# Performance work log

Measured on AMD Instinct MI355X. Metric: run time of the kernel, lower is better.

Reference implementation:

```python
import jax, jax.numpy as jnp
import numpy as np

T, KBLK, EMB, B = 2048, 64, 512, 4


def _make_coords(t, k):
    # head1: for each j, cols = block_start(j) + arange(j % k + 1)  (block-causal local)
    j = np.arange(t)
    cnt1 = (j % k) + 1
    rows1 = np.repeat(j, cnt1)
    off1 = np.arange(cnt1.sum()) - np.repeat(np.cumsum(cnt1) - cnt1, cnt1)
    cols1 = (rows1 // k) * k + off1
    # head2: for each block start c, rows = arange(c, t), col = c  (strided block-start)
    starts = np.arange(t // k) * k
    cnt2 = t - starts
    base = np.repeat(starts, cnt2)
    off2 = np.arange(cnt2.sum()) - np.repeat(np.cumsum(cnt2) - cnt2, cnt2)
    rows2, cols2 = base + off2, base
    c1 = np.stack([rows1, cols1], 1).astype(np.int32)
    c2 = np.stack([rows2, cols2], 1).astype(np.int32)
    return c1, c2


def setup_inputs() -> dict:
    key = jax.random.key(0)
    ks = jax.random.split(key, 6)
    s = 1.0 / float(np.sqrt(EMB))
    c1, c2 = _make_coords(T, KBLK)
    return {
        "x": jax.random.normal(ks[0], (B, T, EMB), jnp.float32),
        "Wk": jax.random.normal(ks[1], (EMB, EMB), jnp.float32) * s,
        "bk": jnp.zeros((EMB,), jnp.float32),
        "Wq": jax.random.normal(ks[2], (EMB, EMB), jnp.float32) * s,
        "bq": jnp.zeros((EMB,), jnp.float32),
        "Wv": jax.random.normal(ks[3], (EMB, EMB), jnp.float32) * s,
        "bv": jnp.zeros((EMB,), jnp.float32),
        "Wu": jax.random.normal(ks[4], (EMB, 2 * EMB), jnp.float32) * s,
        "bu": jnp.zeros((EMB,), jnp.float32),
        "coords1": jnp.asarray(c1),
        "coords2": jnp.asarray(c2),
    }


def _sparse_head(Kt, Qt, Vt, coords):
    rows, cols = coords[:, 0], coords[:, 1]
    # dot[b,p] = (K @ Q^T)[b, rows[p], cols[p]] = K[b,rows[p],:] . Q[b,cols[p],:]
    dot = jnp.einsum('bpe,bpe->bp', Kt[:, rows], Qt[:, cols])
    # sparse.batchmm: out[b,r] = sum_{p: rows[p]=r} dot[b,p] * V[b, cols[p]]
    out = jnp.zeros_like(Vt).at[:, rows].add(dot[..., None] * Vt[:, cols])
    return out


def reference(x, Wk, bk, Wq, bq, Wv, bv, Wu, bu, coords1, coords2):
    Kt = x @ Wk.T + bk
    Qt = x @ Wq.T + bq
    Vt = x @ Wv.T + bv
    h1 = _sparse_head(Kt, Qt, Vt, coords1)
    h2 = _sparse_head(Kt, Qt, Vt, coords2)
    comb = jnp.concatenate([h1, h2], axis=-1)  # [B, T, 2*EMB]
    return comb @ Wu.T + bu
```

## Files before the change

kernel.cpp:

```cpp
#include <hip/hip_runtime.h>


typedef unsigned short u16;
typedef __attribute__((ext_vector_type(8))) short short8;
typedef __attribute__((ext_vector_type(4))) float f32x4;

constexpr int TDIM  = 2048;
constexpr int EMB_D = 512;
constexpr int BB    = 4;
constexpr int NBLK  = 32;
constexpr int LDK   = 2048;

__device__ __forceinline__ u16 f2b(float f) {
    unsigned u = __float_as_uint(f);
    unsigned r = (u + 0x7FFFu + ((u >> 16) & 1u)) >> 16;
    return (u16)r;
}

__global__ __launch_bounds__(256) void prep_k(
    const float* __restrict__ x, const float* __restrict__ Wk, const float* __restrict__ Wq,
    const float* __restrict__ Wv, const float* __restrict__ Wu,
    const float* __restrict__ bk, const float* __restrict__ bq, const float* __restrict__ bv,
    u16* __restrict__ xb, u16* __restrict__ wcat, float* __restrict__ biascat)
{
    const int bid = blockIdx.x, tid = threadIdx.x;
    if (bid < 32) {
        const int bm = (bid >> 2) * 128;
        const int bn = (bid & 3) * 128;
        const int wid  = tid >> 6;
        const int lane = tid & 63;
        const int l15  = lane & 15;
        const int quad = lane >> 4;
        const int wm = (wid & 1) * 64;
        const int wn = (wid >> 1) * 64;

        f32x4 acc[4][4] = {};

        const float* Arow[4];
        #pragma unroll
        for (int i = 0; i < 4; ++i) {
            const int m = bm + wm + 16 * i + l15;
            Arow[i] = Wu + (size_t)(m & 511) * 1024 + (m >> 9) * 512 + quad * 8;
        }
        const float* Bcol[4];
        #pragma unroll
        for (int g = 0; g < 4; ++g)
            Bcol[g] = Wv + (bn + wn + 16 * g + l15) + (size_t)(quad * 8) * 512;

        for (int j0 = 0; j0 < 512; j0 += 32) {
            short8 a[4], b[4];
            #pragma unroll
            for (int i = 0; i < 4; ++i) {
                float4 v0 = *(const float4*)(Arow[i] + j0);
                float4 v1 = *(const float4*)(Arow[i] + j0 + 4);
                a[i] = (short8){(short)f2b(v0.x), (short)f2b(v0.y), (short)f2b(v0.z), (short)f2b(v0.w),
                                (short)f2b(v1.x), (short)f2b(v1.y), (short)f2b(v1.z), (short)f2b(v1.w)};
            }
            #pragma unroll
            for (int g = 0; g < 4; ++g) {
                const float* p = Bcol[g] + (size_t)j0 * 512;
                float v0 = p[0];          float v1 = p[512];
                float v2 = p[1024];       float v3 = p[1536];
                float v4 = p[2048];       float v5 = p[2560];
                float v6 = p[3072];       float v7 = p[3584];
                b[g] = (short8){(short)f2b(v0), (short)f2b(v1), (short)f2b(v2), (short)f2b(v3),
                                (short)f2b(v4), (short)f2b(v5), (short)f2b(v6), (short)f2b(v7)};
            }
            #pragma unroll
            for (int i = 0; i < 4; ++i)
                #pragma unroll
                for (int g = 0; g < 4; ++g)
                    acc[i][g] = __builtin_amdgcn_mfma_f32_16x16x32_bf16(a[i], b[g], acc[i][g], 0, 0, 0);
        }

        #pragma unroll
        for (int i = 0; i < 4; ++i)
            #pragma unroll
            for (int g = 0; g < 4; ++g) {
                const int col = bn + wn + 16 * g + l15;
                #pragma unroll
                for (int r = 0; r < 4; ++r) {
                    const int row = bm + wm + 16 * i + quad * 4 + r;
                    wcat[(size_t)(1024 + row) * 512 + col] = f2b(acc[i][g][r]);
                }
            }
    } else if (bid < 608) {
        const float* src; u16* dst; int base;
        if (bid < 544)      { src = x;  dst = xb;            base = (bid - 32) * 8192; }
        else if (bid < 576) { src = Wk; dst = wcat;          base = (bid - 544) * 8192; }
        else                { src = Wq; dst = wcat + 262144; base = (bid - 576) * 8192; }
        #pragma unroll
        for (int it = 0; it < 8; ++it) {
            const int idx = base + it * 1024 + tid * 4;
            float4 v = *(const float4*)(src + idx);
            ushort4 o = { f2b(v.x), f2b(v.y), f2b(v.z), f2b(v.w) };
            *(ushort4*)(dst + idx) = o;
        }
    } else if (bid < 624) {
        const int o = (bid - 608) * 64 + (tid >> 2);
        const int p = tid & 3;
        const int n = o & 511, half = o >> 9;
        const float* wr = Wu + (size_t)n * 1024 + half * 512 + p * 128;
        const float* br = bv + p * 128;
        float s = 0.f;
        #pragma unroll
        for (int j = 0; j < 128; j += 4) {
            float4 a = *(const float4*)(wr + j);
            float4 b = *(const float4*)(br + j);
            s += a.x*b.x + a.y*b.y + a.z*b.z + a.w*b.w;
        }
        s += __shfl_xor(s, 1);
        s += __shfl_xor(s, 2);
        if (p == 0) biascat[1024 + o] = s;
    } else {
        const int idx = tid * 4;
        float4 v = (idx < 512) ? *(const float4*)(bk + idx)
                               : *(const float4*)(bq + idx - 512);
        *(float4*)(biascat + idx) = v;
    }
}

template<int MH, int KK>
__device__ __forceinline__ void mm16(const short8 (&a)[4], const short8 (&b)[2][4],
                                     f32x4 (&acc)[8][4])
{
    #pragma unroll
    for (int f = 0; f < 4; ++f)
        #pragma unroll
        for (int g = 0; g < 4; ++g)
            acc[MH * 4 + f][g] = __builtin_amdgcn_mfma_f32_16x16x32_bf16(
                a[f], b[KK][g], acc[MH * 4 + f][g], 0, 0, 0);
}

template<int SLOT, int MH>
__device__ __forceinline__ void lda4(short8 (&a)[4], const u16* sm, int arow, int koff)
{
    #pragma unroll
    for (int f = 0; f < 4; ++f)
        a[f] = *(const short8*)(sm + SLOT * 32768 + (arow + MH * 64 + f * 16) * 64 + koff);
}

template<int SLOT>
__device__ __forceinline__ void ldb4(short8 (&bk)[4], const u16* sm, int brow, int koff)
{
    #pragma unroll
    for (int g = 0; g < 4; ++g)
        bk[g] = *(const short8*)(sm + SLOT * 32768 + 16384 + (brow + g * 16) * 64 + koff);
}

#define STA(S, CI, T) __builtin_amdgcn_global_load_lds( \
    (const __attribute__((address_space(1))) void*)(Ag + (size_t)(CI) * 32768 + (T) * 64), \
    (__attribute__((address_space(3))) void*)(sm + (S) * 32768 + (CI) * 4096 + wid * 512), 16, 0, 0)
#define STB(S, CI, T) __builtin_amdgcn_global_load_lds( \
    (const __attribute__((address_space(1))) void*)(Bg + (size_t)(CI) * 32768 + (T) * 64), \
    (__attribute__((address_space(3))) void*)(sm + (S) * 32768 + 16384 + (CI) * 4096 + wid * 512), 16, 0, 0)
#define KBAR()  __builtin_amdgcn_s_barrier()
#define KPRIO(P) __builtin_amdgcn_s_setprio(P)
#define LGKM0() do { asm volatile("s_waitcnt lgkmcnt(0)" ::: "memory"); \
                     __builtin_amdgcn_sched_barrier(0); } while (0)
#define VMC4()  asm volatile("s_waitcnt vmcnt(4)" ::: "memory")
#define VMC0()  asm volatile("s_waitcnt vmcnt(0)" ::: "memory")

__global__ __launch_bounds__(512, 2) void kqv_gemm_k(
    const u16* __restrict__ A, const u16* __restrict__ W,
    const float* __restrict__ bias, u16* __restrict__ C)
{
    __shared__ u16 sm[65536];

    const int bid = blockIdx.x;
    const int wg  = (bid & 7) * 32 + (bid >> 3);
    const int bm  = ((wg >> 3) & 31) * 256;
    const int bn  = (wg & 7) * 256;
    const int tid  = threadIdx.x;
    const int wid  = tid >> 6;
    const int lane = tid & 63;
    const int l15  = lane & 15;
    const int quad = lane >> 4;
    const int wm = wid >> 2;
    const int wn = wid & 3;

    const int stgrow = wid * 8 + (lane >> 3);
    const int stgk   = ((lane & 7) ^ ((lane >> 3) & 7)) << 3;
    const u16* Ag = A + (size_t)(bm + stgrow) * 512 + stgk;
    const u16* Bg = W + (size_t)(bn + stgrow) * 512 + stgk;

    const int r7     = l15 & 7;
    const int arow   = wm * 128 + l15;
    const int brow   = wn * 64 + l15;
    const int off_k0 = ((quad ^ r7) << 3);
    const int off_k1 = (((4 | quad) ^ r7) << 3);

    f32x4 acc[8][4] = {};
    short8 a[4], b[2][4];

    STA(0,0,0); STA(0,2,0); STB(0,0,0); STB(0,1,0);
    STB(0,2,0); STB(0,3,0); STA(0,1,0); STA(0,3,0);
    STA(1,0,1); STA(1,2,1); STB(1,0,1); STB(1,1,1);
    VMC4(); KBAR();

    for (int it = 0; it < 3; ++it) {
        const int t = 2 * it;
        ldb4<0>(b[0], sm, brow, off_k0); lda4<0,0>(a, sm, arow, off_k0);
        STB(1,2,t+1); STB(1,3,t+1);
        KBAR(); LGKM0(); KPRIO(1); mm16<0,0>(a, b, acc); KPRIO(0); KBAR();
        ldb4<0>(b[1], sm, brow, off_k1); lda4<0,0>(a, sm, arow, off_k1);
        STA(1,1,t+1); STA(1,3,t+1);
        KBAR(); LGKM0(); KPRIO(1); mm16<0,1>(a, b, acc); KPRIO(0); KBAR();
        lda4<0,1>(a, sm, arow, off_k0);
        STA(0,0,t+2); STA(0,2,t+2);
        KBAR(); LGKM0(); KPRIO(1); mm16<1,0>(a, b, acc); KPRIO(0); KBAR();
        lda4<0,1>(a, sm, arow, off_k1);
        STB(0,0,t+2); STB(0,1,t+2);
        KBAR(); LGKM0(); KPRIO(1); mm16<1,1>(a, b, acc); KPRIO(0); VMC4(); KBAR();
        ldb4<1>(b[0], sm, brow, off_k0); lda4<1,0>(a, sm, arow, off_k0);
        STB(0,2,t+2); STB(0,3,t+2);
        KBAR(); LGKM0(); KPRIO(1); mm16<0,0>(a, b, acc); KPRIO(0); KBAR();
        ldb4<1>(b[1], sm, brow, off_k1); lda4<1,0>(a, sm, arow, off_k1);
        STA(0,1,t+2); STA(0,3,t+2);
        KBAR(); LGKM0(); KPRIO(1); mm16<0,1>(a, b, acc); KPRIO(0); KBAR();
        lda4<1,1>(a, sm, arow, off_k0);
        STA(1,0,t+3); STA(1,2,t+3);
        KBAR(); LGKM0(); KPRIO(1); mm16<1,0>(a, b, acc); KPRIO(0); KBAR();
        lda4<1,1>(a, sm, arow, off_k1);
        STB(1,0,t+3); STB(1,1,t+3);
        KBAR(); LGKM0(); KPRIO(1); mm16<1,1>(a, b, acc); KPRIO(0); VMC4(); KBAR();
    }

    ldb4<0>(b[0], sm, brow, off_k0); lda4<0,0>(a, sm, arow, off_k0);
    STB(1,2,7); STB(1,3,7);
    KBAR(); LGKM0(); KPRIO(1); mm16<0,0>(a, b, acc); KPRIO(0); KBAR();
    ldb4<0>(b[1], sm, brow, off_k1); lda4<0,0>(a, sm, arow, off_k1);
    STA(1,1,7); STA(1,3,7);
    KBAR(); LGKM0(); KPRIO(1); mm16<0,1>(a, b, acc); KPRIO(0); KBAR();
    lda4<0,1>(a, sm, arow, off_k0);
    KBAR(); LGKM0(); KPRIO(1); mm16<1,0>(a, b, acc); KPRIO(0); KBAR();
    lda4<0,1>(a, sm, arow, off_k1);
    KBAR(); LGKM0(); KPRIO(1); mm16<1,1>(a, b, acc); KPRIO(0); VMC0(); KBAR();
    ldb4<1>(b[0], sm, brow, off_k0); lda4<1,0>(a, sm, arow, off_k0);
    KBAR(); LGKM0(); KPRIO(1); mm16<0,0>(a, b, acc); KPRIO(0); KBAR();
    ldb4<1>(b[1], sm, brow, off_k1); lda4<1,0>(a, sm, arow, off_k1);
    KBAR(); LGKM0(); KPRIO(1); mm16<0,1>(a, b, acc); KPRIO(0); KBAR();
    lda4<1,1>(a, sm, arow, off_k0);
    KBAR(); LGKM0(); KPRIO(1); mm16<1,0>(a, b, acc); KPRIO(0); KBAR();
    lda4<1,1>(a, sm, arow, off_k1);
    KBAR(); LGKM0(); KPRIO(1); mm16<1,1>(a, b, acc); KPRIO(0);

    __syncthreads();
    #pragma unroll
    for (int mf = 0; mf < 8; ++mf) {
        #pragma unroll
        for (int g = 0; g < 4; ++g) {
            const int col = wn * 64 + g * 16 + l15;
            const float bvv = bias[bn + col];
            #pragma unroll
            for (int r = 0; r < 4; ++r) {
                const int row = wm * 128 + mf * 16 + quad * 4 + r;
                sm[row * 256 + col] = f2b(acc[mf][g][r] + bvv);
            }
        }
    }
    __syncthreads();
    {
        const int rr = tid >> 5;
        const int ck = tid & 31;
        #pragma unroll
        for (int p = 0; p < 16; ++p) {
            const int row = p * 16 + rr;
            short8 v = *(const short8*)(sm + row * 256 + ck * 8);
            *(short8*)(C + (size_t)(bm + row) * LDK + bn + ck * 8) = v;
        }
    }
}

#undef STA
#undef STB
#undef KBAR
#undef KPRIO
#undef LGKM0
#undef VMC4
#undef VMC0

__global__ __launch_bounds__(512) void heads_k(
    const u16* __restrict__ KQV, const float* __restrict__ bu, float* __restrict__ out)
{
    __shared__ u16 smA[64 * 104];
    __shared__ u16 smVT[256 * 104];
    __shared__ u16 pK[2][64 * 32];
    __shared__ u16 pQ[2][64 * 32];
    __shared__ u16 pQs[2][32 * 32];

    const int blk = blockIdx.x, b = blockIdx.y;
    const int e0 = blockIdx.z * 256;
    const int tid = threadIdx.x;
    const int wid = tid >> 6, lane = tid & 63;
    const int l15 = lane & 15, quad = lane >> 4;
    const int rw = wid & 3, ch = wid >> 2;
    const size_t row0 = (size_t)b * TDIM + (size_t)blk * 64;
    const size_t brow = (size_t)b * TDIM;
    const int srow_base = 16 * rw + quad * 4;

    #pragma unroll
    for (int it = 0; it < 4; ++it) {
        const int id = tid + 512 * it;
        const int c  = id & 63;
        const int eo = (id >> 6) * 8;
        short8 v = *(const short8*)(KQV + (row0 + c) * (size_t)LDK + 1024 + e0 + eo);
        #pragma unroll
        for (int i = 0; i < 8; ++i) smVT[(eo + i) * 104 + c] = (u16)v[i];
    }
    #pragma unroll
    for (int it = 0; it < 2; ++it) {
        const int id = tid + 512 * it;
        const int m  = id & 31;
        const int eo = (id >> 5) * 8;
        short8 v = *(const short8*)(KQV + (brow + 64 * m) * (size_t)LDK + 1536 + e0 + eo);
        #pragma unroll
        for (int i = 0; i < 8; ++i) smVT[(eo + i) * 104 + 64 + m] = (u16)v[i];
    }

    f32x4 s1[2] = {}; f32x4 s2 = {};
    const int strow  = (tid >> 2) & 63;
    const int sthalf = tid >> 8;
    const int stk    = (tid & 3) * 8;
    const u16* Kg = KQV + (row0 + strow) * (size_t)LDK + sthalf * 32 + stk;
    const u16* Qg = Kg + 512;
    const int qrow  = (tid >> 2) & 31;
    const int qhalf = (tid >> 7) & 1;
    const u16* Qsg = KQV + (brow + (size_t)64 * qrow) * (size_t)LDK + 512 + qhalf * 32 + stk;
    char* dK  = (char*)pK  + wid * 1024;
    char* dQ  = (char*)pQ  + wid * 1024;
    char* dQs = (char*)pQs + wid * 1024;

    for (int k0 = 0; k0 < 512; k0 += 64) {
        __syncthreads();
        __builtin_amdgcn_global_load_lds(
            (const __attribute__((address_space(1))) void*)(Kg + k0),
            (__attribute__((address_space(3))) void*)dK, 16, 0, 0);
        __builtin_amdgcn_global_load_lds(
            (const __attribute__((address_space(1))) void*)(Qg + k0),
            (__attribute__((address_space(3))) void*)dQ, 16, 0, 0);
        if (wid < 4)
            __builtin_amdgcn_global_load_lds(
                (const __attribute__((address_space(1))) void*)(Qsg + k0),
                (__attribute__((address_space(3))) void*)dQs, 16, 0, 0);
        __syncthreads();

        short8 a0 = *(const short8*)(pK[0] + (16 * rw + l15) * 32 + quad * 8);
        short8 a1 = *(const short8*)(pK[1] + (16 * rw + l15) * 32 + quad * 8);
        #pragma unroll
        for (int jj = 0; jj < 2; ++jj) {
            const int j = 2 * ch + jj;
            short8 b0 = *(const short8*)(pQ[0] + (16 * j + l15) * 32 + quad * 8);
            short8 b1 = *(const short8*)(pQ[1] + (16 * j + l15) * 32 + quad * 8);
            s1[jj] = __builtin_amdgcn_mfma_f32_16x16x32_bf16(a0, b0, s1[jj], 0, 0, 0);
            s1[jj] = __builtin_amdgcn_mfma_f32_16x16x32_bf16(a1, b1, s1[jj], 0, 0, 0);
        }
        {
            short8 b0 = *(const short8*)(pQs[0] + (16 * ch + l15) * 32 + quad * 8);
            short8 b1 = *(const short8*)(pQs[1] + (16 * ch + l15) * 32 + quad * 8);
            s2 = __builtin_amdgcn_mfma_f32_16x16x32_bf16(a0, b0, s2, 0, 0, 0);
            s2 = __builtin_amdgcn_mfma_f32_16x16x32_bf16(a1, b1, s2, 0, 0, 0);
        }
    }

    #pragma unroll
    for (int jj = 0; jj < 2; ++jj)
        #pragma unroll
        for (int r = 0; r < 4; ++r) {
            const int rr = srow_base + r;
            const int cc = 32 * ch + 16 * jj + l15;
            smA[rr * 104 + cc] = f2b((cc <= rr) ? s1[jj][r] : 0.0f);
        }
    #pragma unroll
    for (int r = 0; r < 4; ++r) {
        const int m  = 16 * ch + l15;
        const int rr = srow_base + r;
        smA[rr * 104 + 64 + m] = f2b((m <= blk) ? s2[r] : 0.0f);
    }
    __syncthreads();

    f32x4 o[8] = {};
    const u16* arow = smA + (16 * rw + l15) * 104;
    #pragma unroll
    for (int ks = 0; ks < 3; ++ks) {
        short8 as = *(const short8*)(arow + 32 * ks + quad * 8);
        #pragma unroll
        for (int nt = 0; nt < 8; ++nt) {
            short8 bs = *(const short8*)(smVT + (16 * (8 * ch + nt) + l15) * 104 + 32 * ks + quad * 8);
            o[nt] = __builtin_amdgcn_mfma_f32_16x16x32_bf16(as, bs, o[nt], 0, 0, 0);
        }
    }
    #pragma unroll
    for (int nt = 0; nt < 8; ++nt) {
        const int col = e0 + 16 * (8 * ch + nt) + l15;
        const float bvv = bu[col];
        #pragma unroll
        for (int r = 0; r < 4; ++r)
            out[(row0 + srow_base + r) * (size_t)EMB_D + col] = o[nt][r] + bvv;
    }
}

extern "C" void kernel_launch(void* const* d_in, const int* in_sizes, int n_in,
                              void* d_out, int out_size, void* d_ws, size_t ws_size,
                              hipStream_t stream)
{
    const float* x  = (const float*)d_in[0];
    const float* Wk = (const float*)d_in[1];
    const float* bk = (const float*)d_in[2];
    const float* Wq = (const float*)d_in[3];
    const float* bq = (const float*)d_in[4];
    const float* Wv = (const float*)d_in[5];
    const float* bv = (const float*)d_in[6];
    const float* Wu = (const float*)d_in[7];
    const float* bu = (const float*)d_in[8];
    float* out = (float*)d_out;

    char* w = (char*)d_ws;
    u16*   KQV     = (u16*)  (w + ((size_t)0  << 20));
    u16*   xb      = (u16*)  (w + ((size_t)32 << 20));
    u16*   wcat    = (u16*)  (w + ((size_t)40 << 20));
    float* biascat = (float*)(w + ((size_t)44 << 20));

    hipLaunchKernelGGL(prep_k, dim3(625), dim3(256), 0, stream,
                       x, Wk, Wq, Wv, Wu, bk, bq, bv, xb, wcat, biascat);
    hipLaunchKernelGGL(kqv_gemm_k, dim3(256), dim3(512), 0, stream, xb, wcat, biascat, KQV);
    hipLaunchKernelGGL(heads_k, dim3(NBLK, BB, 2), dim3(512), 0, stream, KQV, bu, out);
}
```

Measured before the change: 142.0 us.

## Stage Wu·Wv weight product through double-buffered swizzled LDS

The Wu×Wv precompute GEMM in the prep kernel used to read fp32 operands straight from global memory with strided, uncoalesced column loads. It now streams 32-wide K tiles into double-buffered LDS with global_load_lds, using XOR swizzles, and overlaps the next tile's load with the MFMAs on the current one. This adds 64 KB of static shared memory to the prep kernel, which may cut occupancy for its other conversion branches. Separately, the KQV GEMM's block-to-tile mapping is changed so consecutive workgroups walk along M rather than N, altering L2 reuse.

```diff
diff --git a/kernel.cpp b/kernel.cpp
--- a/kernel.cpp
+++ b/kernel.cpp
@@ -4,6 +4,9 @@
 typedef unsigned short u16;
 typedef __attribute__((ext_vector_type(8))) short short8;
 typedef __attribute__((ext_vector_type(4))) float f32x4;
+
+#define HAS1 __attribute__((address_space(1)))
+#define HAS3 __attribute__((address_space(3)))
 
 constexpr int TDIM  = 2048;
 constexpr int EMB_D = 512;
@@ -23,6 +26,9 @@
     const float* __restrict__ bk, const float* __restrict__ bq, const float* __restrict__ bv,
     u16* __restrict__ xb, u16* __restrict__ wcat, float* __restrict__ biascat)
 {
+    __shared__ float At[2][4096];
+    __shared__ float Bt[2][4096];
+
     const int bid = blockIdx.x, tid = threadIdx.x;
     if (bid < 32) {
         const int bm = (bid >> 2) * 128;
@@ -36,42 +42,70 @@
 
         f32x4 acc[4][4] = {};
 
-        const float* Arow[4];
-        #pragma unroll
-        for (int i = 0; i < 4; ++i) {
-            const int m = bm + wm + 16 * i + l15;
-            Arow[i] = Wu + (size_t)(m & 511) * 1024 + (m >> 9) * 512 + quad * 8;
-        }
-        const float* Bcol[4];
-        #pragma unroll
-        for (int g = 0; g < 4; ++g)
-            Bcol[g] = Wv + (bn + wn + 16 * g + l15) + (size_t)(quad * 8) * 512;
-
-        for (int j0 = 0; j0 < 512; j0 += 32) {
+#define WST(BUF, J0) do { \
+    _Pragma("unroll") \
+    for (int cl = 0; cl < 4; ++cl) { \
+        const int idA = cl * 256 + tid; \
+        const int rA  = idA >> 3; \
+        const int cAx = (idA & 7) ^ (rA & 7); \
+        const int mA  = bm + rA; \
+        __builtin_amdgcn_global_load_lds( \
+            (const HAS1 void*)(Wu + (size_t)(mA & 511) * 1024 + (mA >> 9) * 512 + (J0) + cAx * 4), \
+            (HAS3 void*)((char*)At + (BUF) * 16384 + (idA & 0x3C0) * 16), 16, 0, 0); \
+        const int rB  = idA >> 5; \
+        const int cBx = (idA & 31) ^ ((rB >> 3) << 2); \
+        __builtin_amdgcn_global_load_lds( \
+            (const HAS1 void*)(Wv + (size_t)((J0) + rB) * 512 + bn + cBx * 4), \
+            (HAS3 void*)((char*)Bt + (BUF) * 16384 + (idA & 0x3C0) * 16), 16, 0, 0); \
+    } \
+} while (0)
+
+        WST(0, 0);
+        for (int t = 0; t < 16; ++t) {
+            const int buf = t & 1;
+            if (t < 15) {
+                WST(buf ^ 1, (t + 1) * 32);
+                asm volatile("s_waitcnt vmcnt(8)" ::: "memory");
+            } else {
+                asm volatile("s_waitcnt vmcnt(0)" ::: "memory");
+            }
+            __builtin_amdgcn_s_barrier();
+            __builtin_amdgcn_sched_barrier(0);
+
+            const float* Ab = &At[buf][0];
+            const float* Bb = &Bt[buf][0];
             short8 a[4], b[4];
             #pragma unroll
             for (int i = 0; i < 4; ++i) {
-                float4 v0 = *(const float4*)(Arow[i] + j0);
-                float4 v1 = *(const float4*)(Arow[i] + j0 + 4);
+                const int ml = wm + 16 * i + l15;
+                const float* pa = Ab + ml * 32;
+                const int x0 = (((quad * 2)     ^ (ml & 7)) << 2);
+                const int x1 = (((quad * 2 + 1) ^ (ml & 7)) << 2);
+                float4 v0 = *(const float4*)(pa + x0);
+                float4 v1 = *(const float4*)(pa + x1);
                 a[i] = (short8){(short)f2b(v0.x), (short)f2b(v0.y), (short)f2b(v0.z), (short)f2b(v0.w),
                                 (short)f2b(v1.x), (short)f2b(v1.y), (short)f2b(v1.z), (short)f2b(v1.w)};
             }
             #pragma unroll
             for (int g = 0; g < 4; ++g) {
-                const float* p = Bcol[g] + (size_t)j0 * 512;
-                float v0 = p[0];          float v1 = p[512];
-                float v2 = p[1024];       float v3 = p[1536];
-                float v4 = p[2048];       float v5 = p[2560];
-                float v6 = p[3072];       float v7 = p[3584];
-                b[g] = (short8){(short)f2b(v0), (short)f2b(v1), (short)f2b(v2), (short)f2b(v3),
-                                (short)f2b(v4), (short)f2b(v5), (short)f2b(v6), (short)f2b(v7)};
+                const int c  = wn + 16 * g + l15;
+                const int pc = ((((c >> 2) ^ (quad << 2))) << 2) + (c & 3);
+                const float* pb = Bb + quad * 8 * 128 + pc;
+                float t0 = pb[0];       float t1 = pb[128];
+                float t2 = pb[256];     float t3 = pb[384];
+                float t4 = pb[512];     float t5 = pb[640];
+                float t6 = pb[768];     float t7 = pb[896];
+                b[g] = (short8){(short)f2b(t0), (short)f2b(t1), (short)f2b(t2), (short)f2b(t3),
+                                (short)f2b(t4), (short)f2b(t5), (short)f2b(t6), (short)f2b(t7)};
             }
             #pragma unroll
             for (int i = 0; i < 4; ++i)
                 #pragma unroll
                 for (int g = 0; g < 4; ++g)
                     acc[i][g] = __builtin_amdgcn_mfma_f32_16x16x32_bf16(a[i], b[g], acc[i][g], 0, 0, 0);
-        }
+            __builtin_amdgcn_s_barrier();
+        }
+#undef WST
 
         #pragma unroll
         for (int i = 0; i < 4; ++i)
@@ -149,11 +183,11 @@
 }
 
 #define STA(S, CI, T) __builtin_amdgcn_global_load_lds( \
-    (const __attribute__((address_space(1))) void*)(Ag + (size_t)(CI) * 32768 + (T) * 64), \
-    (__attribute__((address_space(3))) void*)(sm + (S) * 32768 + (CI) * 4096 + wid * 512), 16, 0, 0)
+    (const HAS1 void*)(Ag + (size_t)(CI) * 32768 + (T) * 64), \
+    (HAS3 void*)(sm + (S) * 32768 + (CI) * 4096 + wid * 512), 16, 0, 0)
 #define STB(S, CI, T) __builtin_amdgcn_global_load_lds( \
-    (const __attribute__((address_space(1))) void*)(Bg + (size_t)(CI) * 32768 + (T) * 64), \
-    (__attribute__((address_space(3))) void*)(sm + (S) * 32768 + 16384 + (CI) * 4096 + wid * 512), 16, 0, 0)
+    (const HAS1 void*)(Bg + (size_t)(CI) * 32768 + (T) * 64), \
+    (HAS3 void*)(sm + (S) * 32768 + 16384 + (CI) * 4096 + wid * 512), 16, 0, 0)
 #define KBAR()  __builtin_amdgcn_s_barrier()
 #define KPRIO(P) __builtin_amdgcn_s_setprio(P)
 #define LGKM0() do { asm volatile("s_waitcnt lgkmcnt(0)" ::: "memory"); \
@@ -169,8 +203,8 @@
 
     const int bid = blockIdx.x;
     const int wg  = (bid & 7) * 32 + (bid >> 3);
-    const int bm  = ((wg >> 3) & 31) * 256;
-    const int bn  = (wg & 7) * 256;
+    const int bm  = (wg & 31) * 256;
+    const int bn  = (wg >> 5) * 256;
     const int tid  = threadIdx.x;
     const int wid  = tid >> 6;
     const int lane = tid & 63;
@@ -334,15 +368,15 @@
     for (int k0 = 0; k0 < 512; k0 += 64) {
         __syncthreads();
         __builtin_amdgcn_global_load_lds(
-            (const __attribute__((address_space(1))) void*)(Kg + k0),
-            (__attribute__((address_space(3))) void*)dK, 16, 0, 0);
+            (const HAS1 void*)(Kg + k0),
+            (HAS3 void*)dK, 16, 0, 0);
         __builtin_amdgcn_global_load_lds(
-            (const __attribute__((address_space(1))) void*)(Qg + k0),
-            (__attribute__((address_space(3))) void*)dQ, 16, 0, 0);
+            (const HAS1 void*)(Qg + k0),
+            (HAS3 void*)dQ, 16, 0, 0);
         if (wid < 4)
             __builtin_amdgcn_global_load_lds(
-                (const __attribute__((address_space(1))) void*)(Qsg + k0),
-                (__attribute__((address_space(3))) void*)dQs, 16, 0, 0);
+                (const HAS1 void*)(Qsg + k0),
+                (HAS3 void*)dQs, 16, 0, 0);
         __syncthreads();
 
         short8 a0 = *(const short8*)(pK[0] + (16 * rw + l15) * 32 + quad * 8);
```

Result: no change. 141.3 us (-0.5%).
